# Kernel tuning notes

Hardware: AMD Instinct MI355X
Metric: run time of the kernel (lower is better)

Reference implementation:

```python
import jax, jax.numpy as jnp
import numpy as np

HEAD_DIM = 64

def setup_inputs() -> dict:
    key = jax.random.key(0)
    k1, k2, k3, k4 = jax.random.split(key, 4)
    B, T, C, D = 8, 2048, 1024, HEAD_DIM
    x = jax.random.normal(k1, (B, T, C), dtype=jnp.float32)
    Wq = jax.random.normal(k2, (C, D), dtype=jnp.float32) * (1.0 / np.sqrt(C))
    Wk = jax.random.normal(k3, (C, D), dtype=jnp.float32) * (1.0 / np.sqrt(C))
    Wv = jax.random.normal(k4, (C, D), dtype=jnp.float32) * (1.0 / np.sqrt(C))
    return {"x": x, "Wq": Wq, "Wk": Wk, "Wv": Wv}

def reference(x, Wq, Wk, Wv):
    B, T, C = x.shape
    D = Wq.shape[1]
    q = jnp.einsum('btc,cd->btd', x, Wq)
    k = jnp.einsum('btc,cd->btd', x, Wk)
    v = jnp.einsum('btc,cd->btd', x, Wv)
    scale = 1.0 / jnp.sqrt(jnp.asarray(D, dtype=x.dtype))
    wei = jnp.einsum('bqd,bkd->bqk', q, k) * scale  # [B,T,T]
    causal = jnp.tril(jnp.ones((T, T), dtype=bool))
    wei = jnp.where(causal[None, :, :], wei, -jnp.inf)
    wei = jax.nn.softmax(wei, axis=-1)
    # dropout p=0.0 (eval) -> identity
    out = jnp.einsum('bqk,bkd->bqd', wei, v)  # [B,T,D]
    return out
```

## Files before the change

### kernel.cpp

```cpp
#include <hip/hip_runtime.h>
#include <hip/hip_bf16.h>


typedef __attribute__((ext_vector_type(8))) short short8;
typedef __attribute__((ext_vector_type(4))) float f32x4;

#define MFMA16(a, b, c) __builtin_amdgcn_mfma_f32_16x16x32_bf16((a), (b), (c), 0, 0, 0)

__device__ __forceinline__ unsigned short f2bf(float f) {
  unsigned int u = __builtin_bit_cast(unsigned int, f);
  unsigned int r = 0x7fffu + ((u >> 16) & 1u);
  return (unsigned short)((u + r) >> 16);
}

#define BATCH 8
#define SEQ   2048
#define CDIM  1024
#define DDIM  64
#define NTOK  (BATCH * SEQ)
#define LOG2E 1.44269504f

__global__ __launch_bounds__(256) void wt_kernel(const float* __restrict__ Wq,
                                                 const float* __restrict__ Wk,
                                                 const float* __restrict__ Wv,
                                                 unsigned short* __restrict__ WT) {
  int tid = blockIdx.x * 256 + threadIdx.x;
  int c    = tid & 63;
  int rest = tid >> 6;
  int k    = rest & 1023;
  int wi   = rest >> 10;
  const float* W = (wi == 0) ? Wq : ((wi == 1) ? Wk : Wv);
  float v = W[k * DDIM + c];
  if (wi == 0) v *= 0.125f * LOG2E;
  int row  = wi * 64 + c;
  int step = k >> 6;
  int col  = k & 63;
  size_t idx = (size_t)step * 12288 + (size_t)row * 64 +
               (size_t)(((col >> 3) ^ (row & 7)) * 8) + (col & 7);
  WT[idx] = f2bf(v);
}

__global__ __launch_bounds__(512) void proj_kernel(const float* __restrict__ x,
                                                   const unsigned short* __restrict__ WT,
                                                   unsigned short* __restrict__ qws,
                                                   unsigned short* __restrict__ kws,
                                                   unsigned short* __restrict__ vtws) {
  __shared__ __align__(16) unsigned short xs[2][32 * 64];
  __shared__ __align__(16) unsigned short wl[2][192 * 64];

  const int tid  = threadIdx.x;
  const int lane = tid & 63;
  const int w    = tid >> 6;
  const int wm   = w & 1;
  const int wn   = w >> 1;
  const int c16  = lane & 15;
  const int hi   = lane >> 4;
  const int n0   = blockIdx.x * 32;
  const bool xldr = (tid < 256);
  const int trow = (tid >> 3) & 31;
  const int kch  = tid & 7;

  f32x4 acc[3];
#pragma unroll
  for (int ct = 0; ct < 3; ++ct) acc[ct] = (f32x4){0.f, 0.f, 0.f, 0.f};

  const float* xbase = x + (size_t)(n0 + trow) * CDIM + kch * 8;
  const int xsw = trow * 64 + ((kch ^ (trow & 7)) * 8);

  const unsigned short* wsrc = WT + (size_t)w * 1536 + (size_t)lane * 8;
  auto stage_wt = [&](int step, int bufi) {
    const unsigned short* s = wsrc + (size_t)step * 12288;
    unsigned short* d = &wl[bufi][w * 1536];
#pragma unroll
    for (int j = 0; j < 3; ++j)
      __builtin_amdgcn_global_load_lds(
          (const __attribute__((address_space(1))) void*)(s + j * 512),
          (__attribute__((address_space(3))) void*)(d + j * 512), 16, 0, 0);
  };
  auto xstore = [&](f32x4 a, f32x4 b, int bufi) {
    short8 h;
#pragma unroll
    for (int j = 0; j < 4; ++j) { h[j] = (short)f2bf(a[j]); h[4 + j] = (short)f2bf(b[j]); }
    *reinterpret_cast<short8*>(&xs[bufi][xsw]) = h;
  };

  f32x4 xa1 = {0,0,0,0}, xb1 = xa1, xa2 = xa1, xb2 = xa1;
  if (xldr) {
    f32x4 a0 = *reinterpret_cast<const f32x4*>(xbase);
    f32x4 b0 = *reinterpret_cast<const f32x4*>(xbase + 4);
    xstore(a0, b0, 0);
    xa1 = *reinterpret_cast<const f32x4*>(xbase + 64);
    xb1 = *reinterpret_cast<const f32x4*>(xbase + 64 + 4);
  }
  stage_wt(0, 0);
  __syncthreads();

  int cur = 0;
  for (int st = 0; st < 16; ++st) {
    if (st + 2 < 16 && xldr) {
      xa2 = *reinterpret_cast<const f32x4*>(xbase + (st + 2) * 64);
      xb2 = *reinterpret_cast<const f32x4*>(xbase + (st + 2) * 64 + 4);
    }
    if (st + 1 < 16) stage_wt(st + 1, cur ^ 1);

    short8 bfrag[2];
    {
      int r = wm * 16 + c16;
#pragma unroll
      for (int f = 0; f < 2; ++f)
        bfrag[f] = *reinterpret_cast<const short8*>(
            &xs[cur][r * 64 + (((f * 4 + hi) ^ (r & 7)) * 8)]);
    }
#pragma unroll
    for (int ct = 0; ct < 3; ++ct) {
      int ra = (wn * 3 + ct) * 16 + c16;
#pragma unroll
      for (int f = 0; f < 2; ++f) {
        short8 af = *reinterpret_cast<const short8*>(
            &wl[cur][ra * 64 + (((f * 4 + hi) ^ (ra & 7)) * 8)]);
        acc[ct] = MFMA16(af, bfrag[f], acc[ct]);
      }
    }

    if (st + 1 < 16 && xldr) xstore(xa1, xb1, cur ^ 1);
    __syncthreads();
    xa1 = xa2; xb1 = xb2;
    cur ^= 1;
  }

  {
    const int token = n0 + wm * 16 + c16;
    const int b = token >> 11;
    const int t = token & 2047;
#pragma unroll
    for (int ct = 0; ct < 3; ++ct) {
      int cg = (wn * 3 + ct) * 16 + hi * 4;
      unsigned short h[4];
#pragma unroll
      for (int r = 0; r < 4; ++r) h[r] = f2bf(acc[ct][r]);
      if (cg < 64) {
        *reinterpret_cast<ushort4*>(qws + (size_t)token * DDIM + cg) =
            make_ushort4(h[0], h[1], h[2], h[3]);
      } else if (cg < 128) {
        *reinterpret_cast<ushort4*>(kws + (size_t)token * DDIM + (cg - 64)) =
            make_ushort4(h[0], h[1], h[2], h[3]);
      } else {
        int cv = cg - 128;
#pragma unroll
        for (int r = 0; r < 4; ++r)
          vtws[(size_t)(b * DDIM + cv + r) * SEQ + t] = h[r];
      }
    }
  }
}

__global__ __launch_bounds__(256) void attn_partial(const unsigned short* __restrict__ qws,
                                                    const unsigned short* __restrict__ kws,
                                                    const unsigned short* __restrict__ vtws,
                                                    float* __restrict__ po,
                                                    float* __restrict__ pml,
                                                    int MAXCH, int CHUNK) {
  __shared__ __align__(16) unsigned short kt[2][64 * 64];
  __shared__ __align__(16) unsigned short vt[2][64 * 64];
  __shared__ unsigned short pt[4][64 * 26];

  const int qt = blockIdx.x;
  const int ch = blockIdx.y;
  const int b  = blockIdx.z;

  const int kv_end = qt * 64 + 64;
  const int kv0_ch = ch * CHUNK;
  if (kv0_ch >= kv_end) return;
  const int block_lim = min(kv0_ch + CHUNK, kv_end);
  const int nt = (block_lim - kv0_ch + 63) >> 6;

  const int tid  = threadIdx.x;
  const int lane = tid & 63;
  const int w    = tid >> 6;
  const int c    = lane & 15;
  const int hi   = lane >> 4;
  const int qr0  = qt * 64 + w * 16;
  const int q    = qr0 + c;
  const int kv_last = qr0 + 15;

  const unsigned short* qb = qws + (size_t)b * SEQ * DDIM;
  short8 aq0 = *reinterpret_cast<const short8*>(qb + (size_t)q * DDIM + hi * 8);
  short8 aq1 = *reinterpret_cast<const short8*>(qb + (size_t)q * DDIM + 32 + hi * 8);

  float m = -INFINITY, l = 0.f;
  f32x4 o[4];
#pragma unroll
  for (int dn = 0; dn < 4; ++dn) o[dn] = (f32x4){0.f, 0.f, 0.f, 0.f};

  unsigned short* pw = pt[w];
  const unsigned short* kb = kws + (size_t)b * SEQ * DDIM;
  const unsigned short* vb = vtws + (size_t)b * DDIM * SEQ;

  auto stage_kv = [&](int bufi, int kv0) {
#pragma unroll
    for (int j = 0; j < 2; ++j) {
      int p   = w * 128 + j * 64 + lane;
      int row = p >> 3;
      int chk = (p & 7) ^ (row & 7);
      __builtin_amdgcn_global_load_lds(
          (const __attribute__((address_space(1))) void*)(kb + (size_t)(kv0 + row) * DDIM + chk * 8),
          (__attribute__((address_space(3))) void*)(&kt[bufi][w * 1024 + j * 512]), 16, 0, 0);
      __builtin_amdgcn_global_load_lds(
          (const __attribute__((address_space(1))) void*)(vb + (size_t)row * SEQ + kv0 + chk * 8),
          (__attribute__((address_space(3))) void*)(&vt[bufi][w * 1024 + j * 512]), 16, 0, 0);
    }
  };

  stage_kv(0, kv0_ch);
  __syncthreads();

  int cur = 0;
  for (int t = 0; t < nt; ++t) {
    const int kv0 = kv0_ch + t * 64;
    if (t + 1 < nt) stage_kv(cur ^ 1, kv0 + 64);

    if (kv0 <= kv_last) {
      f32x4 s[4];
#pragma unroll
      for (int n = 0; n < 4; ++n) {
        if (kv0 + n * 16 > kv_last) {
          s[n] = (f32x4){-INFINITY, -INFINITY, -INFINITY, -INFINITY};
          continue;
        }
        const unsigned short* kr = &kt[cur][(n * 16 + c) * 64];
        short8 ka0 = *reinterpret_cast<const short8*>(kr + ((hi ^ (c & 7)) * 8));
        short8 ka1 = *reinterpret_cast<const short8*>(kr + (((4 + hi) ^ (c & 7)) * 8));
        f32x4 z = (f32x4){0.f, 0.f, 0.f, 0.f};
        z = MFMA16(ka0, aq0, z);
        s[n] = MFMA16(ka1, aq1, z);
      }

      if (kv0 + 63 > qr0) {
#pragma unroll
        for (int n = 0; n < 4; ++n)
#pragma unroll
          for (int r = 0; r < 4; ++r)
            if (kv0 + n * 16 + hi * 4 + r > q) s[n][r] = -INFINITY;
      }

      float mx = -INFINITY;
#pragma unroll
      for (int n = 0; n < 4; ++n)
        mx = fmaxf(mx, fmaxf(fmaxf(s[n][0], s[n][1]), fmaxf(s[n][2], s[n][3])));
      mx = fmaxf(mx, __shfl_xor(mx, 16, 64));
      mx = fmaxf(mx, __shfl_xor(mx, 32, 64));

      float nm = fmaxf(m, mx);
      float sc = __builtin_exp2f(m - nm);
      m = nm;

      float ssum = 0.f;
#pragma unroll
      for (int n = 0; n < 4; ++n)
#pragma unroll
        for (int r = 0; r < 4; ++r) {
          float pv = __builtin_exp2f(s[n][r] - nm);
          pw[(n * 16 + hi * 4 + r) * 26 + c] = f2bf(pv);
          ssum += pv;
        }
      ssum += __shfl_xor(ssum, 16, 64);
      ssum += __shfl_xor(ssum, 32, 64);
      l = l * sc + ssum;

#pragma unroll
      for (int dn = 0; dn < 4; ++dn) o[dn] *= sc;

      const int nf = (kv0 + 32 <= kv_last) ? 2 : 1;
      for (int f = 0; f < nf; ++f) {
        short8 bp;
#pragma unroll
        for (int j = 0; j < 8; ++j)
          bp[j] = (short)pw[(f * 32 + hi * 8 + j) * 26 + c];
#pragma unroll
        for (int dn = 0; dn < 4; ++dn) {
          const unsigned short* vr = &vt[cur][(dn * 16 + c) * 64];
          short8 va = *reinterpret_cast<const short8*>(vr + (((f * 4 + hi) ^ (c & 7)) * 8));
          o[dn] = MFMA16(va, bp, o[dn]);
        }
      }
    }

    __syncthreads();
    cur ^= 1;
  }

  float* pob = po + (((size_t)(b * 32 + qt) * MAXCH + ch) * 64 + w * 16 + c) * 64 + hi * 4;
#pragma unroll
  for (int dn = 0; dn < 4; ++dn)
    *reinterpret_cast<f32x4*>(pob + dn * 16) = o[dn];

  if (hi == 0) {
    *reinterpret_cast<float2*>(
        pml + (((size_t)(b * 32 + qt) * MAXCH + ch) * 64 + w * 16 + c) * 2) =
        make_float2(m, l);
  }
}

__global__ __launch_bounds__(256) void attn_combine(const float* __restrict__ po,
                                                    const float* __restrict__ pml,
                                                    float* __restrict__ out,
                                                    int MAXCH, int CHUNK) {
  const int qt = blockIdx.x;
  const int b  = blockIdx.y;
  const int tid = threadIdx.x;
  const int row = tid >> 2;
  const int cg  = tid & 3;
  const int nch = (qt * 64 + 64 + CHUNK - 1) / CHUNK;

  const size_t base = (size_t)(b * 32 + qt) * MAXCH;

  float M = -INFINITY;
  for (int ch = 0; ch < nch; ++ch)
    M = fmaxf(M, pml[(base + ch) * 128 + row * 2]);

  float L = 0.f;
  f32x4 a0 = {0.f,0.f,0.f,0.f}, a1 = a0, a2 = a0, a3 = a0;
  for (int ch = 0; ch < nch; ++ch) {
    float mv = pml[(base + ch) * 128 + row * 2];
    float lv = pml[(base + ch) * 128 + row * 2 + 1];
    float wgt = __builtin_exp2f(mv - M);
    L += wgt * lv;
    const float* p = po + (base + ch) * 4096 + row * 64 + cg * 16;
    a0 += wgt * *reinterpret_cast<const f32x4*>(p);
    a1 += wgt * *reinterpret_cast<const f32x4*>(p + 4);
    a2 += wgt * *reinterpret_cast<const f32x4*>(p + 8);
    a3 += wgt * *reinterpret_cast<const f32x4*>(p + 12);
  }
  float invL = 1.f / L;
  float* ob = out + ((size_t)b * SEQ + qt * 64 + row) * 64 + cg * 16;
  *reinterpret_cast<f32x4*>(ob)      = a0 * invL;
  *reinterpret_cast<f32x4*>(ob + 4)  = a1 * invL;
  *reinterpret_cast<f32x4*>(ob + 8)  = a2 * invL;
  *reinterpret_cast<f32x4*>(ob + 12) = a3 * invL;
}

extern "C" void kernel_launch(void* const* d_in, const int* in_sizes, int n_in,
                              void* d_out, int out_size, void* d_ws, size_t ws_size,
                              hipStream_t stream) {
  const float* x  = (const float*)d_in[0];
  const float* Wq = (const float*)d_in[1];
  const float* Wk = (const float*)d_in[2];
  const float* Wv = (const float*)d_in[3];
  float* out = (float*)d_out;

  unsigned short* qws  = (unsigned short*)d_ws;
  unsigned short* kws  = qws + (size_t)NTOK * DDIM;
  unsigned short* vtws = kws + (size_t)NTOK * DDIM;
  unsigned short* WT   = vtws + (size_t)NTOK * DDIM;
  size_t fixed_end = (size_t)NTOK * DDIM * 3 * 2 + 192 * 1024 * 2;

  int MAXCH = 1;
  {
    const int cand[4] = {8, 4, 2, 1};
    for (int i = 0; i < 4; ++i) {
      size_t need = fixed_end +
                    (size_t)cand[i] * (8ull * 32 * 64 * 64 * 4 + 8ull * 32 * 64 * 2 * 4);
      if (need <= ws_size) { MAXCH = cand[i]; break; }
    }
  }

  wt_kernel<<<768, 256, 0, stream>>>(Wq, Wk, Wv, WT);
  proj_kernel<<<NTOK / 32, 512, 0, stream>>>(x, WT, qws, kws, vtws);

  float* po  = (float*)((char*)d_ws + fixed_end);
  float* pml = po + (size_t)BATCH * 32 * MAXCH * 64 * 64;
  int CHUNK = SEQ / MAXCH;
  attn_partial<<<dim3(32, MAXCH, BATCH), 256, 0, stream>>>(qws, kws, vtws, po, pml,
                                                           MAXCH, CHUNK);
  attn_combine<<<dim3(32, BATCH), 256, 0, stream>>>(po, pml, out, MAXCH, CHUNK);
}
```

Baseline: 65.80 us.

## Triple-buffer projection and attention loads with explicit waitcnt barriers

The projection kernel moves to three weight LDS buffers. All 512 threads now load x, each taking four floats, with a prefetch depth of two. The plain __syncthreads calls are replaced by s_waitcnt vmcnt/lgkmcnt and s_barrier, so later loads can stay in flight across the barrier. The attention partial kernel gets the same triple buffering for K/V tiles with counted vmcnt waits, and the combine kernel unrolls its chunk loop to at most 8 chunks with hoisted m/l loads. The larger LDS footprint may lower occupancy. The hand-set vmcnt counts and the 8-chunk cap depend on MAXCH ≤ 8 and on the exact number of outstanding loads.

Measured after the change: 70.81 us. 7.6% more time.

```diff
diff --git a/kernel.cpp b/kernel.cpp
--- a/kernel.cpp
+++ b/kernel.cpp
@@ -46,7 +46,7 @@
                                                    unsigned short* __restrict__ kws,
                                                    unsigned short* __restrict__ vtws) {
   __shared__ __align__(16) unsigned short xs[2][32 * 64];
-  __shared__ __align__(16) unsigned short wl[2][192 * 64];
+  __shared__ __align__(16) unsigned short wl[3][192 * 64];
 
   const int tid  = threadIdx.x;
   const int lane = tid & 63;
@@ -56,16 +56,17 @@
   const int c16  = lane & 15;
   const int hi   = lane >> 4;
   const int n0   = blockIdx.x * 32;
-  const bool xldr = (tid < 256);
-  const int trow = (tid >> 3) & 31;
-  const int kch  = tid & 7;
+
+  const int xrow = tid >> 4;
+  const int xq4  = tid & 15;
+  const int xch  = xq4 >> 1;
+  const int xhf  = xq4 & 1;
+  const float* xsrc = x + (size_t)(n0 + xrow) * CDIM + xq4 * 4;
+  const int xdst = xrow * 64 + ((xch ^ (xrow & 7)) * 8) + xhf * 4;
 
   f32x4 acc[3];
 #pragma unroll
   for (int ct = 0; ct < 3; ++ct) acc[ct] = (f32x4){0.f, 0.f, 0.f, 0.f};
-
-  const float* xbase = x + (size_t)(n0 + trow) * CDIM + kch * 8;
-  const int xsw = trow * 64 + ((kch ^ (trow & 7)) * 8);
 
   const unsigned short* wsrc = WT + (size_t)w * 1536 + (size_t)lane * 8;
   auto stage_wt = [&](int step, int bufi) {
@@ -77,31 +78,26 @@
           (const __attribute__((address_space(1))) void*)(s + j * 512),
           (__attribute__((address_space(3))) void*)(d + j * 512), 16, 0, 0);
   };
-  auto xstore = [&](f32x4 a, f32x4 b, int bufi) {
-    short8 h;
-#pragma unroll
-    for (int j = 0; j < 4; ++j) { h[j] = (short)f2bf(a[j]); h[4 + j] = (short)f2bf(b[j]); }
-    *reinterpret_cast<short8*>(&xs[bufi][xsw]) = h;
+  auto xwrite = [&](f32x4 v, int bufi) {
+    ushort4 h = make_ushort4(f2bf(v[0]), f2bf(v[1]), f2bf(v[2]), f2bf(v[3]));
+    *reinterpret_cast<ushort4*>(&xs[bufi][xdst]) = h;
   };
 
-  f32x4 xa1 = {0,0,0,0}, xb1 = xa1, xa2 = xa1, xb2 = xa1;
-  if (xldr) {
-    f32x4 a0 = *reinterpret_cast<const f32x4*>(xbase);
-    f32x4 b0 = *reinterpret_cast<const f32x4*>(xbase + 4);
-    xstore(a0, b0, 0);
-    xa1 = *reinterpret_cast<const f32x4*>(xbase + 64);
-    xb1 = *reinterpret_cast<const f32x4*>(xbase + 64 + 4);
-  }
   stage_wt(0, 0);
-  __syncthreads();
-
-  int cur = 0;
+  asm volatile("s_waitcnt vmcnt(0)" ::: "memory");
+  f32x4 xv = *reinterpret_cast<const f32x4*>(xsrc);
+  xwrite(xv, 0);
+  stage_wt(1, 1);
+  f32x4 xr_w = *reinterpret_cast<const f32x4*>(xsrc + 64);
+  f32x4 xr_a = *reinterpret_cast<const f32x4*>(xsrc + 128);
+  asm volatile("s_waitcnt lgkmcnt(0)" ::: "memory");
+  __builtin_amdgcn_s_barrier();
+
+  int wcur = 0, wstg = 2;
   for (int st = 0; st < 16; ++st) {
-    if (st + 2 < 16 && xldr) {
-      xa2 = *reinterpret_cast<const f32x4*>(xbase + (st + 2) * 64);
-      xb2 = *reinterpret_cast<const f32x4*>(xbase + (st + 2) * 64 + 4);
-    }
-    if (st + 1 < 16) stage_wt(st + 1, cur ^ 1);
+    if (st <= 13) stage_wt(st + 2, wstg);
+    f32x4 xr_b;
+    if (st <= 12) xr_b = *reinterpret_cast<const f32x4*>(xsrc + (st + 3) * 64);
 
     short8 bfrag[2];
     {
@@ -109,7 +105,7 @@
 #pragma unroll
       for (int f = 0; f < 2; ++f)
         bfrag[f] = *reinterpret_cast<const short8*>(
-            &xs[cur][r * 64 + (((f * 4 + hi) ^ (r & 7)) * 8)]);
+            &xs[st & 1][r * 64 + (((f * 4 + hi) ^ (r & 7)) * 8)]);
     }
 #pragma unroll
     for (int ct = 0; ct < 3; ++ct) {
@@ -117,15 +113,23 @@
 #pragma unroll
       for (int f = 0; f < 2; ++f) {
         short8 af = *reinterpret_cast<const short8*>(
-            &wl[cur][ra * 64 + (((f * 4 + hi) ^ (ra & 7)) * 8)]);
+            &wl[wcur][ra * 64 + (((f * 4 + hi) ^ (ra & 7)) * 8)]);
         acc[ct] = MFMA16(af, bfrag[f], acc[ct]);
       }
     }
 
-    if (st + 1 < 16 && xldr) xstore(xa1, xb1, cur ^ 1);
-    __syncthreads();
-    xa1 = xa2; xb1 = xb2;
-    cur ^= 1;
+    if (st <= 14) xwrite(xr_w, (st + 1) & 1);
+
+    if (st < 15) {
+      asm volatile("s_waitcnt lgkmcnt(0)" ::: "memory");
+      if (st <= 12)      asm volatile("s_waitcnt vmcnt(4)" ::: "memory");
+      else if (st == 13) asm volatile("s_waitcnt vmcnt(3)" ::: "memory");
+      else               asm volatile("s_waitcnt vmcnt(0)" ::: "memory");
+      __builtin_amdgcn_s_barrier();
+    }
+    xr_w = xr_a; xr_a = xr_b;
+    wcur = (wcur == 2) ? 0 : wcur + 1;
+    wstg = (wstg == 2) ? 0 : wstg + 1;
   }
 
   {
@@ -160,8 +164,8 @@
                                                     float* __restrict__ po,
                                                     float* __restrict__ pml,
                                                     int MAXCH, int CHUNK) {
-  __shared__ __align__(16) unsigned short kt[2][64 * 64];
-  __shared__ __align__(16) unsigned short vt[2][64 * 64];
+  __shared__ __align__(16) unsigned short kt[3][64 * 64];
+  __shared__ __align__(16) unsigned short vt[3][64 * 64];
   __shared__ unsigned short pt[4][64 * 26];
 
   const int qt = blockIdx.x;
@@ -212,12 +216,21 @@
   };
 
   stage_kv(0, kv0_ch);
-  __syncthreads();
-
-  int cur = 0;
+  if (nt > 1) {
+    stage_kv(1, kv0_ch + 64);
+    asm volatile("s_waitcnt vmcnt(4)" ::: "memory");
+  } else {
+    asm volatile("s_waitcnt vmcnt(0)" ::: "memory");
+  }
+  __builtin_amdgcn_s_barrier();
+
+  int bufc = 0;
   for (int t = 0; t < nt; ++t) {
     const int kv0 = kv0_ch + t * 64;
-    if (t + 1 < nt) stage_kv(cur ^ 1, kv0 + 64);
+    if (t + 2 < nt) {
+      int bstg = bufc + 2; if (bstg >= 3) bstg -= 3;
+      stage_kv(bstg, kv0 + 128);
+    }
 
     if (kv0 <= kv_last) {
       f32x4 s[4];
@@ -227,7 +240,7 @@
           s[n] = (f32x4){-INFINITY, -INFINITY, -INFINITY, -INFINITY};
           continue;
         }
-        const unsigned short* kr = &kt[cur][(n * 16 + c) * 64];
+        const unsigned short* kr = &kt[bufc][(n * 16 + c) * 64];
         short8 ka0 = *reinterpret_cast<const short8*>(kr + ((hi ^ (c & 7)) * 8));
         short8 ka1 = *reinterpret_cast<const short8*>(kr + (((4 + hi) ^ (c & 7)) * 8));
         f32x4 z = (f32x4){0.f, 0.f, 0.f, 0.f};
@@ -278,15 +291,19 @@
           bp[j] = (short)pw[(f * 32 + hi * 8 + j) * 26 + c];
 #pragma unroll
         for (int dn = 0; dn < 4; ++dn) {
-          const unsigned short* vr = &vt[cur][(dn * 16 + c) * 64];
+          const unsigned short* vr = &vt[bufc][(dn * 16 + c) * 64];
           short8 va = *reinterpret_cast<const short8*>(vr + (((f * 4 + hi) ^ (c & 7)) * 8));
           o[dn] = MFMA16(va, bp, o[dn]);
         }
       }
     }
 
-    __syncthreads();
-    cur ^= 1;
+    if (t < nt - 1) {
+      if (t + 2 < nt) asm volatile("s_waitcnt vmcnt(4)" ::: "memory");
+      else            asm volatile("s_waitcnt vmcnt(0)" ::: "memory");
+      __builtin_amdgcn_s_barrier();
+    }
+    bufc = (bufc == 2) ? 0 : bufc + 1;
   }
 
   float* pob = po + (((size_t)(b * 32 + qt) * MAXCH + ch) * 64 + w * 16 + c) * 64 + hi * 4;
@@ -310,27 +327,35 @@
   const int tid = threadIdx.x;
   const int row = tid >> 2;
   const int cg  = tid & 3;
-  const int nch = (qt * 64 + 64 + CHUNK - 1) / CHUNK;
+  const int nch = min((qt * 64 + 64 + CHUNK - 1) / CHUNK, MAXCH);
 
   const size_t base = (size_t)(b * 32 + qt) * MAXCH;
 
-  float M = -INFINITY;
-  for (int ch = 0; ch < nch; ++ch)
-    M = fmaxf(M, pml[(base + ch) * 128 + row * 2]);
+  float mv0 = -INFINITY, mv1 = -INFINITY, mv2 = -INFINITY, mv3 = -INFINITY;
+  float mv4 = -INFINITY, mv5 = -INFINITY, mv6 = -INFINITY, mv7 = -INFINITY;
+  float lv0 = 0, lv1 = 0, lv2 = 0, lv3 = 0, lv4 = 0, lv5 = 0, lv6 = 0, lv7 = 0;
+#define LOADML(i) if (i < nch) { \
+    float2 t = *reinterpret_cast<const float2*>(pml + (base + i) * 128 + row * 2); \
+    mv##i = t.x; lv##i = t.y; }
+  LOADML(0) LOADML(1) LOADML(2) LOADML(3) LOADML(4) LOADML(5) LOADML(6) LOADML(7)
+#undef LOADML
+
+  float M = fmaxf(fmaxf(fmaxf(mv0, mv1), fmaxf(mv2, mv3)),
+                  fmaxf(fmaxf(mv4, mv5), fmaxf(mv6, mv7)));
 
   float L = 0.f;
   f32x4 a0 = {0.f,0.f,0.f,0.f}, a1 = a0, a2 = a0, a3 = a0;
-  for (int ch = 0; ch < nch; ++ch) {
-    float mv = pml[(base + ch) * 128 + row * 2];
-    float lv = pml[(base + ch) * 128 + row * 2 + 1];
-    float wgt = __builtin_exp2f(mv - M);
-    L += wgt * lv;
-    const float* p = po + (base + ch) * 4096 + row * 64 + cg * 16;
-    a0 += wgt * *reinterpret_cast<const f32x4*>(p);
-    a1 += wgt * *reinterpret_cast<const f32x4*>(p + 4);
-    a2 += wgt * *reinterpret_cast<const f32x4*>(p + 8);
-    a3 += wgt * *reinterpret_cast<const f32x4*>(p + 12);
-  }
+#define ACC(i) if (i < nch) { \
+    float wgt = __builtin_exp2f(mv##i - M); \
+    L += wgt * lv##i; \
+    const float* p = po + (base + i) * 4096 + row * 64 + cg * 16; \
+    a0 += wgt * *reinterpret_cast<const f32x4*>(p); \
+    a1 += wgt * *reinterpret_cast<const f32x4*>(p + 4); \
+    a2 += wgt * *reinterpret_cast<const f32x4*>(p + 8); \
+    a3 += wgt * *reinterpret_cast<const f32x4*>(p + 12); }
+  ACC(0) ACC(1) ACC(2) ACC(3) ACC(4) ACC(5) ACC(6) ACC(7)
+#undef ACC
+
   float invL = 1.f / L;
   float* ob = out + ((size_t)b * SEQ + qt * 64 + row) * 64 + cg * 16;
   *reinterpret_cast<f32x4*>(ob)      = a0 * invL;
```
